# Optimization experiments

Hardware: AMD Instinct MI355X
Metric: run time of the kernel (lower is better)

The kernel has to match this reference:

```python
import jax, jax.numpy as jnp
import numpy as np

B, T, C = 4, 1024, 1024
HEAD_SIZE = 64
H = C // HEAD_SIZE
N_LAYER, LAYER_ID = 24, 12
D_MIX_LORA, D_DECAY_LORA = 32, 64
HEAD_SIZE_DIVISOR = 8
LN_EPS = 1e-5 * HEAD_SIZE_DIVISOR ** 2


def setup_inputs() -> dict:
    key = jax.random.key(0)
    ks = jax.random.split(key, 16)
    x = jax.random.normal(ks[0], (B, T, C), jnp.float32)

    r01 = LAYER_ID / (N_LAYER - 1)          # ratio_0_to_1
    r10 = 1.0 - LAYER_ID / N_LAYER          # ratio_1_to_almost0
    ddd = np.arange(C, dtype=np.float64) / C

    time_maa_x = jnp.asarray((1.0 - ddd ** r10).astype(np.float32))
    time_maa_w = jnp.asarray((1.0 - ddd ** r10).astype(np.float32))
    time_maa_k = jnp.asarray((1.0 - ddd ** r10).astype(np.float32))
    time_maa_v = jnp.asarray((1.0 - (ddd ** r10 + 0.3 * r01)).astype(np.float32))
    time_maa_r = jnp.asarray((1.0 - ddd ** (0.5 * r10)).astype(np.float32))
    time_maa_g = jnp.asarray((1.0 - ddd ** (0.5 * r10)).astype(np.float32))

    n = np.arange(C, dtype=np.float64)
    time_decay = jnp.asarray((-6.0 + 5.0 * (n / (C - 1)) ** (0.7 + 1.3 * r01)).astype(np.float32))
    zigzag = ((n + 1) % 3 - 1) * 0.1
    time_faaaa = jnp.asarray((r01 * (1.0 - n / (C - 1)) + zigzag).astype(np.float32)).reshape(H, HEAD_SIZE)

    u = lambda k, shp: jax.random.uniform(k, shp, jnp.float32, -0.01, 0.01)
    time_maa_w1 = u(ks[1], (C, D_MIX_LORA * 5))   # zeros in orig init; small random for a non-trivial test
    time_maa_w2 = u(ks[2], (5, D_MIX_LORA, C))
    time_decay_w1 = u(ks[3], (C, D_DECAY_LORA))
    time_decay_w2 = u(ks[4], (D_DECAY_LORA, C))

    s = 1.0 / np.sqrt(C)
    Wr = jax.random.normal(ks[5], (C, C), jnp.float32) * s   # stored [in, out]
    Wk = jax.random.normal(ks[6], (C, C), jnp.float32) * s
    Wv = jax.random.normal(ks[7], (C, C), jnp.float32) * s
    Wg = jax.random.normal(ks[8], (C, C), jnp.float32) * s
    Wo = jax.random.normal(ks[9], (C, C), jnp.float32) * s
    ln_w = jnp.ones((C,), jnp.float32)
    ln_b = jnp.zeros((C,), jnp.float32)

    return dict(x=x, time_maa_x=time_maa_x, time_maa_w=time_maa_w, time_maa_k=time_maa_k,
                time_maa_v=time_maa_v, time_maa_r=time_maa_r, time_maa_g=time_maa_g,
                time_maa_w1=time_maa_w1, time_maa_w2=time_maa_w2,
                time_decay=time_decay, time_decay_w1=time_decay_w1, time_decay_w2=time_decay_w2,
                time_faaaa=time_faaaa, Wr=Wr, Wk=Wk, Wv=Wv, Wg=Wg, Wo=Wo, ln_w=ln_w, ln_b=ln_b)


def _wkv6(r, k, v, w, u):
    # r,k,v,w: [B,T,H,N]; u: [H,N]. Data-dependent linear recurrence per head.
    def step(S, inp):               # S: [B,H,N,N] (key dim j, value dim i)
        r_t, k_t, v_t, w_t = inp    # each [B,H,N]
        y = jnp.einsum('bhj,bhji->bhi', r_t, S) \
            + jnp.sum(r_t * u * k_t, axis=-1, keepdims=True) * v_t
        decay = jnp.exp(-jnp.exp(w_t))            # CUDA kernel: w_eff = exp(-exp(w))
        S = decay[..., None] * S + k_t[..., None] * v_t[..., None, :]
        return S, y

    to_t = lambda a: jnp.transpose(a, (1, 0, 2, 3))  # [T,B,H,N]
    S0 = jnp.zeros(r.shape[:1] + (r.shape[2], r.shape[3], r.shape[3]), r.dtype)
    _, ys = jax.lax.scan(step, S0, (to_t(r), to_t(k), to_t(v), to_t(w)))
    return jnp.transpose(ys, (1, 0, 2, 3))            # [B,T,H,N]


def reference(x, time_maa_x, time_maa_w, time_maa_k, time_maa_v, time_maa_r, time_maa_g,
              time_maa_w1, time_maa_w2, time_decay, time_decay_w1, time_decay_w2,
              time_faaaa, Wr, Wk, Wv, Wg, Wo, ln_w, ln_b):
    b, t, c = x.shape
    h, n = H, HEAD_SIZE

    # token shift: ZeroPad2d((0,0,1,-1)) shifts time right by one with zero pad
    xx = jnp.concatenate([jnp.zeros_like(x[:, :1]), x[:, :-1]], axis=1) - x
    xxx = x + xx * time_maa_x
    mix = jnp.tanh(xxx @ time_maa_w1).reshape(b, t, 5, D_MIX_LORA)
    m = jnp.einsum('btsd,sdc->sbtc', mix, time_maa_w2)  # [5,B,T,C]
    xw = x + xx * (time_maa_w + m[0])
    xk = x + xx * (time_maa_k + m[1])
    xv = x + xx * (time_maa_v + m[2])
    xr = x + xx * (time_maa_r + m[3])
    xg = x + xx * (time_maa_g + m[4])

    r = xr @ Wr
    k = xk @ Wk
    v = xv @ Wv
    g = jax.nn.silu(xg @ Wg)
    w = time_decay + jnp.tanh(xw @ time_decay_w1) @ time_decay_w2

    y = _wkv6(r.reshape(b, t, h, n), k.reshape(b, t, h, n),
              v.reshape(b, t, h, n), w.reshape(b, t, h, n), time_faaaa)

    # GroupNorm with n_head groups over channel dim, eps = 1e-5 * divisor^2
    mu = y.mean(-1, keepdims=True)
    var = y.var(-1, keepdims=True)
    yn = ((y - mu) / jnp.sqrt(var + LN_EPS)).reshape(b, t, c) * ln_w + ln_b

    return (yn * g) @ Wo
```

## Files before the change

kernel.cpp:

```cpp
#include <hip/hip_runtime.h>

typedef unsigned short u16;
typedef short short8 __attribute__((ext_vector_type(8)));
typedef short short4v __attribute__((ext_vector_type(4)));
typedef float float4v __attribute__((ext_vector_type(4)));
typedef unsigned uint4v __attribute__((ext_vector_type(4)));

__device__ __forceinline__ float bf2f(u16 h) { return __uint_as_float(((unsigned)h) << 16); }
__device__ __forceinline__ u16 f2bf(float f) {
  unsigned u = __float_as_uint(f);
  unsigned r = (u + 0x7fffu + ((u >> 16) & 1u)) >> 16;
  return (u16)r;
}
__device__ __forceinline__ bool is_f32(const void* probe) {
  return ((const u16*)probe)[0] != 0x3F80;
}
__device__ __forceinline__ float ldin(const void* p, long i, bool f32m) {
  return f32m ? ((const float*)p)[i] : bf2f(((const u16*)p)[i]);
}

typedef __attribute__((address_space(1))) const unsigned int as1_u32;
typedef __attribute__((address_space(3))) unsigned int as3_u32;
__device__ __forceinline__ void gl2lds16(const void* g, void* l) {
  __builtin_amdgcn_global_load_lds((as1_u32*)g, (as3_u32*)l, 16, 0, 0);
}

template <int CTRL>
__device__ __forceinline__ float dpp_add(float x) {
  int s = __builtin_amdgcn_update_dpp(0, __float_as_int(x), CTRL, 0xF, 0xF, true);
  return x + __int_as_float(s);
}

__global__ __launch_bounds__(256) void sentinel_fill(u16* o, long n) {
  long i = (long)blockIdx.x * 256 + threadIdx.x;
  if (i < n) o[i] = 0x42C8;
}

struct TDescArr {
  const void* src[13];
  u16* dst[13];
  int rows[13];
  int cols[13];
  int roff[13];
};

__global__ __launch_bounds__(256) void transpose_all(TDescArr d, const void* probe) {
  bool f32m = is_f32(probe);
  int z = blockIdx.z;
  int rows = d.rows[z], cols = d.cols[z], roff = d.roff[z];
  int bc = blockIdx.x * 32, br = blockIdx.y * 32;
  if (bc >= cols || br >= rows) return;
  const void* src = d.src[z];
  u16* dst = d.dst[z];
  __shared__ u16 tile[32][33];
  int tx = threadIdx.x & 31, ty = threadIdx.x >> 5;
#pragma unroll
  for (int i = 0; i < 32; i += 8)
    tile[ty + i][tx] = f2bf(ldin(src, (long)(roff + br + ty + i) * cols + bc + tx, f32m));
  __syncthreads();
#pragma unroll
  for (int i = 0; i < 32; i += 8)
    dst[(long)(bc + ty + i) * rows + br + tx] = tile[tx][ty + i];
}

__global__ __launch_bounds__(256) void token_shift(const void* __restrict__ x,
                                                   const void* __restrict__ maa_x,
                                                   u16* __restrict__ xxx) {
  bool f32m = is_f32(maa_x);
  long idx = (long)blockIdx.x * 256 + threadIdx.x;
  int c = (int)(idx & 1023);
  int tt = (int)((idx >> 10) & 1023);
  float xv = ldin(x, idx, f32m);
  float xp = tt > 0 ? ldin(x, idx - 1024, f32m) : 0.f;
  xxx[idx] = f2bf(xv + (xp - xv) * ldin(maa_x, c, f32m));
}

template <int EPI>
__global__ __launch_bounds__(256, 2) void gemm_big(const u16* __restrict__ A,
                                                   const u16* __restrict__ Bt,
                                                   void* __restrict__ Cv, int M, int N,
                                                   int K, const void* probe) {
  __shared__ alignas(16) u16 As[128 * 32];
  __shared__ alignas(16) u16 Bs[128 * 32];
  int t = threadIdx.x, lane = t & 63, w = t >> 6;
  int sid = blockIdx.y * gridDim.x + blockIdx.x;
  int per8 = (gridDim.x * gridDim.y) >> 3;
  int L = (sid & 7) * per8 + (sid >> 3);
  int mi = L / gridDim.y, ni = L % gridDim.y;
  int m0 = mi * 128, n0 = ni * 128;
  int wm = (w >> 1) * 64, wn = (w & 1) * 64;
  int lr = lane & 15, lk = lane >> 4;
  float4v acc[4][4];
#pragma unroll
  for (int i = 0; i < 4; i++)
#pragma unroll
    for (int j = 0; j < 4; j++) acc[i][j] = (float4v){0.f, 0.f, 0.f, 0.f};
  const u16* Ag0 = A + (long)(m0 + (t >> 2)) * K + (t & 3) * 8;
  const u16* Ag1 = A + (long)(m0 + 64 + (t >> 2)) * K + (t & 3) * 8;
  const u16* Bg0 = Bt + (long)(n0 + (t >> 2)) * K + (t & 3) * 8;
  const u16* Bg1 = Bt + (long)(n0 + 64 + (t >> 2)) * K + (t & 3) * 8;
  int so = w * 512;
  for (int k0 = 0; k0 < K; k0 += 32) {
    __syncthreads();
    gl2lds16(Ag0 + k0, As + so);
    gl2lds16(Ag1 + k0, As + 2048 + so);
    gl2lds16(Bg0 + k0, Bs + so);
    gl2lds16(Bg1 + k0, Bs + 2048 + so);
    __syncthreads();
    short8 af[4], bfr[4];
#pragma unroll
    for (int i = 0; i < 4; i++)
      af[i] = *(const short8*)(As + (wm + i * 16 + lr) * 32 + lk * 8);
#pragma unroll
    for (int i = 0; i < 4; i++)
      bfr[i] = *(const short8*)(Bs + (wn + i * 16 + lr) * 32 + lk * 8);
#pragma unroll
    for (int mi2 = 0; mi2 < 4; mi2++)
#pragma unroll
      for (int ni2 = 0; ni2 < 4; ni2++)
        acc[mi2][ni2] = __builtin_amdgcn_mfma_f32_16x16x32_bf16(af[mi2], bfr[ni2],
                                                                acc[mi2][ni2], 0, 0, 0);
  }
  bool f32m = (EPI == 2) ? is_f32(probe) : false;
#pragma unroll
  for (int mi2 = 0; mi2 < 4; mi2++) {
#pragma unroll
    for (int ni2 = 0; ni2 < 4; ni2++) {
      int col = n0 + wn + ni2 * 16 + lr;
#pragma unroll
      for (int rr = 0; rr < 4; rr++) {
        long row = m0 + wm + mi2 * 16 + lk * 4 + rr;
        float val = acc[mi2][ni2][rr];
        if (EPI == 1) val = val / (1.f + __expf(-val));
        if (EPI == 2 && f32m) ((float*)Cv)[row * N + col] = val;
        else ((u16*)Cv)[row * N + col] = f2bf(val);
      }
    }
  }
}

template <int EPI0, int EPI1>
__global__ __launch_bounds__(256, 2) void gemm_big2(
    const u16* __restrict__ A0, const u16* __restrict__ Bt0, u16* __restrict__ C0,
    const u16* __restrict__ A1, const u16* __restrict__ Bt1, u16* __restrict__ C1,
    int M, int N, int K) {
  __shared__ alignas(16) u16 As[128 * 32];
  __shared__ alignas(16) u16 Bs[128 * 32];
  int z = blockIdx.z;
  const u16* A = z ? A1 : A0;
  const u16* Bt = z ? Bt1 : Bt0;
  u16* C = z ? C1 : C0;
  int epi = z ? EPI1 : EPI0;
  int t = threadIdx.x, lane = t & 63, w = t >> 6;
  int sid = blockIdx.y * gridDim.x + blockIdx.x;
  int per8 = (gridDim.x * gridDim.y) >> 3;
  int L = (sid & 7) * per8 + (sid >> 3);
  int mi = L / gridDim.y, ni = L % gridDim.y;
  int m0 = mi * 128, n0 = ni * 128;
  int wm = (w >> 1) * 64, wn = (w & 1) * 64;
  int lr = lane & 15, lk = lane >> 4;
  float4v acc[4][4];
#pragma unroll
  for (int i = 0; i < 4; i++)
#pragma unroll
    for (int j = 0; j < 4; j++) acc[i][j] = (float4v){0.f, 0.f, 0.f, 0.f};
  const u16* Ag0 = A + (long)(m0 + (t >> 2)) * K + (t & 3) * 8;
  const u16* Ag1 = A + (long)(m0 + 64 + (t >> 2)) * K + (t & 3) * 8;
  const u16* Bg0 = Bt + (long)(n0 + (t >> 2)) * K + (t & 3) * 8;
  const u16* Bg1 = Bt + (long)(n0 + 64 + (t >> 2)) * K + (t & 3) * 8;
  int so = w * 512;
  for (int k0 = 0; k0 < K; k0 += 32) {
    __syncthreads();
    gl2lds16(Ag0 + k0, As + so);
    gl2lds16(Ag1 + k0, As + 2048 + so);
    gl2lds16(Bg0 + k0, Bs + so);
    gl2lds16(Bg1 + k0, Bs + 2048 + so);
    __syncthreads();
    short8 af[4], bfr[4];
#pragma unroll
    for (int i = 0; i < 4; i++)
      af[i] = *(const short8*)(As + (wm + i * 16 + lr) * 32 + lk * 8);
#pragma unroll
    for (int i = 0; i < 4; i++)
      bfr[i] = *(const short8*)(Bs + (wn + i * 16 + lr) * 32 + lk * 8);
#pragma unroll
    for (int mi2 = 0; mi2 < 4; mi2++)
#pragma unroll
      for (int ni2 = 0; ni2 < 4; ni2++)
        acc[mi2][ni2] = __builtin_amdgcn_mfma_f32_16x16x32_bf16(af[mi2], bfr[ni2],
                                                                acc[mi2][ni2], 0, 0, 0);
  }
#pragma unroll
  for (int mi2 = 0; mi2 < 4; mi2++) {
#pragma unroll
    for (int ni2 = 0; ni2 < 4; ni2++) {
      int col = n0 + wn + ni2 * 16 + lr;
#pragma unroll
      for (int rr = 0; rr < 4; rr++) {
        long row = m0 + wm + mi2 * 16 + lk * 4 + rr;
        float val = acc[mi2][ni2][rr];
        if (epi == 1) val = val / (1.f + __expf(-val));
        C[row * N + col] = f2bf(val);
      }
    }
  }
}

template <int EPI>
__global__ __launch_bounds__(256) void gemm_wave(const u16* __restrict__ A, int lda,
                                                 const u16* __restrict__ Bt,
                                                 u16* __restrict__ C, int ldc,
                                                 float* dA_, float* dB_, int Ntot,
                                                 int K, const void* aux0,
                                                 const void* probe,
                                                 const void* __restrict__ xin) {
  int t = threadIdx.x, lane = t & 63, w = t >> 6;
  int m0 = blockIdx.x * 64 + w * 16;
  int span = Ntot / gridDim.y;
  int col0 = blockIdx.y * span;
  const u16* Bp = Bt + (long)col0 * K;
  int lr = lane & 15, lk = lane >> 4;
  bool f32m = (EPI >= 2) ? is_f32(probe) : false;
  int nt = span >> 4;
  for (int g0 = 0; g0 < nt; g0 += 4) {
    int gc = (nt - g0 < 4) ? (nt - g0) : 4;
    float4v acc[4];
#pragma unroll
    for (int i = 0; i < 4; i++) acc[i] = (float4v){0.f, 0.f, 0.f, 0.f};
    for (int k0 = 0; k0 < K; k0 += 32) {
      short8 a = *(const short8*)(A + (long)(m0 + lr) * lda + k0 + lk * 8);
      for (int gi = 0; gi < gc; gi++) {
        int n0 = (g0 + gi) * 16;
        short8 b = *(const short8*)(Bp + (long)(n0 + lr) * K + k0 + lk * 8);
        acc[gi] = __builtin_amdgcn_mfma_f32_16x16x32_bf16(a, b, acc[gi], 0, 0, 0);
      }
    }
    for (int gi = 0; gi < gc; gi++) {
      int col = col0 + (g0 + gi) * 16 + lr;
      if (EPI == 3) {
        long r0 = m0 + lk * 4;
        float xv4[4];
#pragma unroll
        for (int rr = 0; rr < 4; rr++)
          xv4[rr] = ldin(xin, (r0 + rr) * 1024 + col, f32m);
        float xpv = ((int)(r0 & 1023) > 0) ? ldin(xin, (r0 - 1) * 1024 + col, f32m) : 0.f;
        float mv = ldin(aux0, col, f32m);
#pragma unroll
        for (int rr = 0; rr < 4; rr++) {
          float xv = xv4[rr];
          float xp = (rr == 0) ? xpv : xv4[rr - 1];
          C[(r0 + rr) * 1024 + col] = f2bf(xv + (xp - xv) * (mv + acc[gi][rr]));
        }
      } else {
#pragma unroll
        for (int rr = 0; rr < 4; rr++) {
          long row = m0 + lk * 4 + rr;
          float val = acc[gi][rr];
          if (EPI == 0) {
            C[row * ldc + col] = f2bf(val);
          } else if (EPI == 1) {
            float vv = fminf(fmaxf(val, -15.f), 15.f);
            float e = __expf(2.f * vv);
            C[row * ldc + col] = f2bf((e - 1.f) / (e + 1.f));
          } else if (EPI == 2) {
            float wv = val + ldin(aux0, col, f32m);
            float dv = __expf(-__expf(wv));
            if (row < 2048) dA_[row * 1024 + col] = dv;
            else dB_[(row - 2048) * 1024 + col] = dv;
          }
        }
      }
    }
  }
}

__global__ __launch_bounds__(256) void gemm_wave3_pair(
    const u16* __restrict__ A0, const u16* __restrict__ Bt0, u16* __restrict__ C0,
    const void* __restrict__ maa0, const u16* __restrict__ A1,
    const u16* __restrict__ Bt1, u16* __restrict__ C1,
    const void* __restrict__ maa1, const void* probe,
    const void* __restrict__ xin) {
  int z = blockIdx.z;
  const u16* A = z ? A1 : A0;
  const u16* Bt = z ? Bt1 : Bt0;
  u16* C = z ? C1 : C0;
  const void* maa = z ? maa1 : maa0;
  bool f32m = is_f32(probe);
  int t = threadIdx.x, lane = t & 63, w = t >> 6;
  int m0 = blockIdx.x * 64 + w * 16;
  int col0 = blockIdx.y * 32;
  const u16* Bp = Bt + (long)col0 * 32;
  int lr = lane & 15, lk = lane >> 4;
  float4v acc[2];
  acc[0] = (float4v){0.f, 0.f, 0.f, 0.f};
  acc[1] = (float4v){0.f, 0.f, 0.f, 0.f};
  short8 a = *(const short8*)(A + (long)(m0 + lr) * 160 + lk * 8);
#pragma unroll
  for (int gi = 0; gi < 2; gi++) {
    short8 b = *(const short8*)(Bp + (long)(gi * 16 + lr) * 32 + lk * 8);
    acc[gi] = __builtin_amdgcn_mfma_f32_16x16x32_bf16(a, b, acc[gi], 0, 0, 0);
  }
#pragma unroll
  for (int gi = 0; gi < 2; gi++) {
    int col = col0 + gi * 16 + lr;
    long r0 = m0 + lk * 4;
    float xv4[4];
#pragma unroll
    for (int rr = 0; rr < 4; rr++)
      xv4[rr] = ldin(xin, (r0 + rr) * 1024 + col, f32m);
    float xpv = ((int)(r0 & 1023) > 0) ? ldin(xin, (r0 - 1) * 1024 + col, f32m) : 0.f;
    float mv = ldin(maa, col, f32m);
#pragma unroll
    for (int rr = 0; rr < 4; rr++) {
      float xv = xv4[rr];
      float xp = (rr == 0) ? xpv : xv4[rr - 1];
      C[(r0 + rr) * 1024 + col] = f2bf(xv + (xp - xv) * (mv + acc[gi][rr]));
    }
  }
}

__global__ __launch_bounds__(256) void gemm_n64_tanh(const u16* __restrict__ A,
                                                     const u16* __restrict__ Bt,
                                                     u16* __restrict__ C) {
  int t = threadIdx.x, lane = t & 63, w = t >> 6;
  int m0 = blockIdx.x * 16;
  int n0 = w * 16;
  int lr = lane & 15, lk = lane >> 4;
  float4v acc = (float4v){0.f, 0.f, 0.f, 0.f};
  const u16* Ap = A + (long)(m0 + lr) * 1024;
  const u16* Bp = Bt + (long)(n0 + lr) * 1024;
  for (int k0 = 0; k0 < 1024; k0 += 32) {
    short8 a = *(const short8*)(Ap + k0 + lk * 8);
    short8 b = *(const short8*)(Bp + k0 + lk * 8);
    acc = __builtin_amdgcn_mfma_f32_16x16x32_bf16(a, b, acc, 0, 0, 0);
  }
#pragma unroll
  for (int rr = 0; rr < 4; rr++) {
    long row = m0 + lk * 4 + rr;
    float vv = fminf(fmaxf(acc[rr], -15.f), 15.f);
    float e = __expf(2.f * vv);
    C[row * 64 + n0 + lr] = f2bf((e - 1.f) / (e + 1.f));
  }
}

__global__ __launch_bounds__(256) void wkv6_kernel(
    const u16* __restrict__ r, const u16* __restrict__ k, const u16* __restrict__ v,
    const float* __restrict__ dA_, const float* __restrict__ dB_,
    const void* __restrict__ u_, const void* probe, u16* __restrict__ y) {
  bool f32m = is_f32(probe);
  int bx = blockIdx.x;
  int cb = bx >> 6, bh = bx & 63;
  int b = bh >> 4, h = bh & 15;
  int t = threadIdx.x, lane = t & 63, w = t >> 6;
  int cl = lane >> 3, jq = lane & 7;
  int kp = w * 8 + jq;
  __shared__ alignas(16) uint4v rkd[32][33];
  __shared__ alignas(16) float vsm[8][36];
  __shared__ alignas(16) float ypn[4][8][36];
  float S0 = 0.f, S1 = 0.f;
  float u0 = ldin(u_, h * 64 + 2 * kp, f32m);
  float u1 = ldin(u_, h * 64 + 2 * kp + 1, f32m);
  const long base = ((long)b << 20) + h * 64;
  const float* dgb =
      (b < 2 ? dA_ + (long)b * 1048576 : dB_ + (long)(b - 2) * 1048576) + h * 64;

  int s_tt = t >> 5, s_kp = t & 31;
  int v_tt = t >> 3, v_c = t & 7;

  for (int c0 = 0; c0 < 1024; c0 += 32) {
    {
#pragma unroll
      for (int i = 0; i < 4; i++) {
        int tt = s_tt + i * 8;
        long ro = (long)(c0 + tt) << 10;
        unsigned r2 = *(const unsigned*)(r + base + ro + s_kp * 2);
        unsigned k2 = *(const unsigned*)(k + base + ro + s_kp * 2);
        const float* dp = dgb + ro + s_kp * 2;
        rkd[tt][s_kp] =
            (uint4v){r2, k2, __float_as_uint(dp[0]), __float_as_uint(dp[1])};
      }
      vsm[v_c][v_tt] = bf2f(v[base + ((long)(c0 + v_tt) << 10) + cb * 8 + v_c]);
    }
    __syncthreads();
    float4v vv4;
    float4v yy4;
#pragma unroll
    for (int tt = 0; tt < 32; ++tt) {
      if ((tt & 3) == 0) vv4 = *(const float4v*)&vsm[cl][tt];
      float vt = vv4[tt & 3];
      uint4v q = rkd[tt][kp];
      float r0 = bf2f((u16)(q[0] & 0xffffu)), r1 = bf2f((u16)(q[0] >> 16));
      float k0 = bf2f((u16)(q[1] & 0xffffu)), k1 = bf2f((u16)(q[1] >> 16));
      float d0 = __uint_as_float(q[2]), d1 = __uint_as_float(q[3]);
      float kv0 = k0 * vt, kv1 = k1 * vt;
      float y0 = r0 * fmaf(u0, kv0, S0);
      float y1 = r1 * fmaf(u1, kv1, S1);
      S0 = fmaf(S0, d0, kv0);
      S1 = fmaf(S1, d1, kv1);
      float yy = y0 + y1;
      yy = dpp_add<0xB1>(yy);
      yy = dpp_add<0x4E>(yy);
      yy = dpp_add<0x104>(yy);
      yy4[tt & 3] = yy;
      if ((tt & 3) == 3 && jq == 0)
        *(float4v*)&ypn[w][cl][tt - 3] = yy4;
    }
    __syncthreads();
    {
      int rt = t >> 3, rc = t & 7;
      float s = (ypn[0][rc][rt] + ypn[1][rc][rt]) + (ypn[2][rc][rt] + ypn[3][rc][rt]);
      y[base + ((long)(c0 + rt) << 10) + cb * 8 + rc] = f2bf(s);
    }
    __syncthreads();
  }
}

__global__ __launch_bounds__(256) void gn_gate(const u16* __restrict__ y,
                                               const u16* __restrict__ g,
                                               const void* __restrict__ lnw,
                                               const void* __restrict__ lnb,
                                               const void* probe,
                                               u16* __restrict__ out) {
  bool f32m = is_f32(probe);
  int gid = blockIdx.x * 4 + (threadIdx.x >> 6);
  int lane = threadIdx.x & 63;
  int h = gid & 15;
  long row = gid >> 4;
  long off = row * 1024 + h * 64 + lane;
  float val = bf2f(y[off]);
  float s = val, sq = val * val;
#pragma unroll
  for (int m = 1; m < 64; m <<= 1) {
    s += __shfl_xor(s, m);
    sq += __shfl_xor(sq, m);
  }
  float mean = s * (1.f / 64.f);
  float var = fmaxf(sq * (1.f / 64.f) - mean * mean, 0.f);
  float inv = rsqrtf(var + 6.4e-4f);
  int c = h * 64 + lane;
  float yn = (val - mean) * inv * ldin(lnw, c, f32m) + ldin(lnb, c, f32m);
  out[off] = f2bf(yn * bf2f(g[off]));
}

extern "C" void kernel_launch(void* const* d_in, const int* in_sizes, int n_in,
                              void* d_out, int out_size, void* d_ws, size_t ws_size,
                              hipStream_t stream) {
  const void* x = d_in[0];
  const void* maaX = d_in[1];
  const void* maa_s[5] = {d_in[2], d_in[3], d_in[4], d_in[5], d_in[6]};
  const void* w1 = d_in[7];
  const void* w2 = d_in[8];
  const void* tdec = d_in[9];
  const void* dw1 = d_in[10];
  const void* dw2 = d_in[11];
  const void* faaaa = d_in[12];
  const void* Wr = d_in[13];
  const void* Wk = d_in[14];
  const void* Wv = d_in[15];
  const void* Wg = d_in[16];
  const void* Wo = d_in[17];
  const void* lnw = d_in[18];
  const void* lnb = d_in[19];

  const long oWoT = 4194304;
  const long ow1T = 5242880;
  const long odw1T = 5406720;
  const long odw2T = 5472256;
  const long ow2T = 5537792;
  const long omixb = 5701632;
  const long owtan = 6356992;
  const long oxxxg = 6619136;
  const long omx = 10813440;
  const long orb = 15007744;
  const long okb = 19202048;
  const long ovb = 23396352;
  const long oyb = 27590656;
  const long oend = 31784960;
  const size_t needed = (size_t)oend * 2;

  if (ws_size < needed) {
    sentinel_fill<<<dim3((unsigned)((out_size + 255) / 256)), 256, 0, stream>>>(
        (u16*)d_out, out_size);
    return;
  }

  u16* W = (u16*)d_ws;
  u16* WrT = W;
  u16* WkT = W + 1048576;
  u16* WvT = W + 2097152;
  u16* WgT = W + 3145728;
  u16* WoT = W + oWoT;
  u16* w1T = W + ow1T;
  u16* dw1T = W + odw1T;
  u16* dw2T = W + odw2T;
  u16* w2T = W + ow2T;
  u16* mixb = W + omixb;
  u16* wtan = W + owtan;
  u16* xxxg = W + oxxxg;
  u16* mx = W + omx;
  u16* rbuf = W + orb;
  u16* kbuf = W + okb;
  u16* vbuf = W + ovb;
  u16* ybuf = W + oyb;
  float* dA_ = (float*)W;
  float* dB_ = (float*)(W + omx);
  u16* gated = mx;

  TDescArr td;
  const void* s5[5] = {Wr, Wk, Wv, Wg, Wo};
  u16* t5[5] = {WrT, WkT, WvT, WgT, WoT};
  for (int i = 0; i < 13; i++) td.roff[i] = 0;
  for (int i = 0; i < 5; i++) {
    td.src[i] = s5[i]; td.dst[i] = t5[i]; td.rows[i] = 1024; td.cols[i] = 1024;
  }
  td.src[5] = w1;  td.dst[5] = w1T;  td.rows[5] = 1024; td.cols[5] = 160;
  td.src[6] = dw1; td.dst[6] = dw1T; td.rows[6] = 1024; td.cols[6] = 64;
  td.src[7] = dw2; td.dst[7] = dw2T; td.rows[7] = 64;   td.cols[7] = 1024;
  for (int s = 0; s < 5; s++) {
    td.src[8 + s] = w2;
    td.dst[8 + s] = w2T + s * 1024 * 32;
    td.rows[8 + s] = 32; td.cols[8 + s] = 1024; td.roff[8 + s] = s * 32;
  }

  transpose_all<<<dim3(32, 32, 13), 256, 0, stream>>>(td, maaX);
  token_shift<<<dim3(16384), 256, 0, stream>>>(x, maaX, xxxg);
  gemm_wave<1><<<dim3(64, 10), 256, 0, stream>>>(xxxg, 1024, w1T, mixb, 160, nullptr,
                                                 nullptr, 160, 1024, nullptr, nullptr,
                                                 nullptr);
  gemm_wave3_pair<<<dim3(64, 32, 2), 256, 0, stream>>>(
      mixb + 3 * 32, w2T + 3 * 32768, mx, maa_s[3],
      mixb + 1 * 32, w2T + 1 * 32768, ybuf, maa_s[1], maaX, x);
  gemm_big2<0, 0><<<dim3(32, 8, 2), 256, 0, stream>>>(mx, WrT, rbuf, ybuf, WkT, kbuf,
                                                      4096, 1024, 1024);
  gemm_wave3_pair<<<dim3(64, 32, 2), 256, 0, stream>>>(
      mixb + 2 * 32, w2T + 2 * 32768, mx, maa_s[2],
      mixb + 4 * 32, w2T + 4 * 32768, ybuf, maa_s[4], maaX, x);
  gemm_big2<0, 1><<<dim3(32, 8, 2), 256, 0, stream>>>(mx, WvT, vbuf, ybuf, WgT, xxxg,
                                                      4096, 1024, 1024);
  gemm_wave<3><<<dim3(64, 32), 256, 0, stream>>>(mixb + 0 * 32, 160, w2T + 0 * 32768,
                                                 mx, 1024, nullptr, nullptr, 1024, 32,
                                                 maa_s[0], maaX, x);
  gemm_n64_tanh<<<dim3(256), 256, 0, stream>>>(mx, dw1T, wtan);
  gemm_wave<2><<<dim3(64, 16), 256, 0, stream>>>(wtan, 64, dw2T, nullptr, 0, dA_, dB_,
                                                 1024, 64, tdec, maaX, nullptr);
  wkv6_kernel<<<dim3(512), 256, 0, stream>>>(rbuf, kbuf, vbuf, dA_, dB_, faaaa, maaX,
                                             ybuf);
  gn_gate<<<dim3(16384), 256, 0, stream>>>(ybuf, xxxg, lnw, lnb, maaX, gated);
  gemm_big<2><<<dim3(32, 8), 256, 0, stream>>>(gated, WoT, d_out, 4096, 1024, 1024, maaX);
}
```

Measured before the change: 388.3 us.

## Double GEMM K-tile to 64 with XOR-swizzled LDS and pack WKV math

The shared 128x128 GEMM body is factored into one core routine whose K step grows from 32 to 64. The LDS tile uses an XOR swizzle on the 16-byte chunk index so fragment reads avoid bank conflicts, and half as many barriers run per K. The WKV recurrence is rewritten with two-wide float vectors so the compiler can emit packed FP32 ops, and the bf16 unpack is simplified. The larger LDS tiles (32KB per block) may limit occupancy at two blocks per CU.

After: 378.0 us. 1.03x faster.

```diff
diff --git a/kernel.cpp b/kernel.cpp
--- a/kernel.cpp
+++ b/kernel.cpp
@@ -4,6 +4,7 @@
 typedef short short8 __attribute__((ext_vector_type(8)));
 typedef short short4v __attribute__((ext_vector_type(4)));
 typedef float float4v __attribute__((ext_vector_type(4)));
+typedef float float2v __attribute__((ext_vector_type(2)));
 typedef unsigned uint4v __attribute__((ext_vector_type(4)));
 
 __device__ __forceinline__ float bf2f(u16 h) { return __uint_as_float(((unsigned)h) << 16); }
@@ -76,18 +77,12 @@
 }
 
 template <int EPI>
-__global__ __launch_bounds__(256, 2) void gemm_big(const u16* __restrict__ A,
-                                                   const u16* __restrict__ Bt,
-                                                   void* __restrict__ Cv, int M, int N,
-                                                   int K, const void* probe) {
-  __shared__ alignas(16) u16 As[128 * 32];
-  __shared__ alignas(16) u16 Bs[128 * 32];
+__device__ __forceinline__ void gemm128_core(const u16* __restrict__ A,
+                                             const u16* __restrict__ Bt,
+                                             void* __restrict__ Cv, int N, int K,
+                                             int m0, int n0, u16* As, u16* Bs,
+                                             bool f32m) {
   int t = threadIdx.x, lane = t & 63, w = t >> 6;
-  int sid = blockIdx.y * gridDim.x + blockIdx.x;
-  int per8 = (gridDim.x * gridDim.y) >> 3;
-  int L = (sid & 7) * per8 + (sid >> 3);
-  int mi = L / gridDim.y, ni = L % gridDim.y;
-  int m0 = mi * 128, n0 = ni * 128;
   int wm = (w >> 1) * 64, wn = (w & 1) * 64;
   int lr = lane & 15, lk = lane >> 4;
   float4v acc[4][4];
@@ -95,33 +90,48 @@
   for (int i = 0; i < 4; i++)
 #pragma unroll
     for (int j = 0; j < 4; j++) acc[i][j] = (float4v){0.f, 0.f, 0.f, 0.f};
-  const u16* Ag0 = A + (long)(m0 + (t >> 2)) * K + (t & 3) * 8;
-  const u16* Ag1 = A + (long)(m0 + 64 + (t >> 2)) * K + (t & 3) * 8;
-  const u16* Bg0 = Bt + (long)(n0 + (t >> 2)) * K + (t & 3) * 8;
-  const u16* Bg1 = Bt + (long)(n0 + 64 + (t >> 2)) * K + (t & 3) * 8;
+  int srow = t >> 3;
+  int scol = ((t & 7) ^ (srow & 7)) * 8;
+  const u16* Ag = A + (long)(m0 + srow) * K + scol;
+  const u16* Bg = Bt + (long)(n0 + srow) * K + scol;
   int so = w * 512;
-  for (int k0 = 0; k0 < K; k0 += 32) {
+  for (int k0 = 0; k0 < K; k0 += 64) {
     __syncthreads();
-    gl2lds16(Ag0 + k0, As + so);
-    gl2lds16(Ag1 + k0, As + 2048 + so);
-    gl2lds16(Bg0 + k0, Bs + so);
-    gl2lds16(Bg1 + k0, Bs + 2048 + so);
+#pragma unroll
+    for (int p = 0; p < 4; p++) {
+      gl2lds16(Ag + (long)p * 32 * K + k0, As + p * 2048 + so);
+      gl2lds16(Bg + (long)p * 32 * K + k0, Bs + p * 2048 + so);
+    }
     __syncthreads();
-    short8 af[4], bfr[4];
-#pragma unroll
-    for (int i = 0; i < 4; i++)
-      af[i] = *(const short8*)(As + (wm + i * 16 + lr) * 32 + lk * 8);
-#pragma unroll
-    for (int i = 0; i < 4; i++)
-      bfr[i] = *(const short8*)(Bs + (wn + i * 16 + lr) * 32 + lk * 8);
+    short8 af[4][2], bfr[4][2];
+#pragma unroll
+    for (int i = 0; i < 4; i++) {
+      int R = wm + i * 16 + lr;
+#pragma unroll
+      for (int h = 0; h < 2; h++) {
+        int j = h * 4 + lk;
+        af[i][h] = *(const short8*)(As + R * 64 + (j ^ (R & 7)) * 8);
+      }
+    }
+#pragma unroll
+    for (int i = 0; i < 4; i++) {
+      int R = wn + i * 16 + lr;
+#pragma unroll
+      for (int h = 0; h < 2; h++) {
+        int j = h * 4 + lk;
+        bfr[i][h] = *(const short8*)(Bs + R * 64 + (j ^ (R & 7)) * 8);
+      }
+    }
 #pragma unroll
     for (int mi2 = 0; mi2 < 4; mi2++)
 #pragma unroll
-      for (int ni2 = 0; ni2 < 4; ni2++)
-        acc[mi2][ni2] = __builtin_amdgcn_mfma_f32_16x16x32_bf16(af[mi2], bfr[ni2],
-                                                                acc[mi2][ni2], 0, 0, 0);
-  }
-  bool f32m = (EPI == 2) ? is_f32(probe) : false;
+      for (int ni2 = 0; ni2 < 4; ni2++) {
+        acc[mi2][ni2] = __builtin_amdgcn_mfma_f32_16x16x32_bf16(
+            af[mi2][0], bfr[ni2][0], acc[mi2][ni2], 0, 0, 0);
+        acc[mi2][ni2] = __builtin_amdgcn_mfma_f32_16x16x32_bf16(
+            af[mi2][1], bfr[ni2][1], acc[mi2][ni2], 0, 0, 0);
+      }
+  }
 #pragma unroll
   for (int mi2 = 0; mi2 < 4; mi2++) {
 #pragma unroll
@@ -139,71 +149,37 @@
   }
 }
 
+template <int EPI>
+__global__ __launch_bounds__(256, 2) void gemm_big(const u16* __restrict__ A,
+                                                   const u16* __restrict__ Bt,
+                                                   void* __restrict__ Cv, int M, int N,
+                                                   int K, const void* probe) {
+  __shared__ alignas(16) u16 As[128 * 64];
+  __shared__ alignas(16) u16 Bs[128 * 64];
+  int sid = blockIdx.y * gridDim.x + blockIdx.x;
+  int per8 = (gridDim.x * gridDim.y) >> 3;
+  int L = (sid & 7) * per8 + (sid >> 3);
+  int mi = L / gridDim.y, ni = L % gridDim.y;
+  bool f32m = (EPI == 2) ? is_f32(probe) : false;
+  gemm128_core<EPI>(A, Bt, Cv, N, K, mi * 128, ni * 128, As, Bs, f32m);
+}
+
 template <int EPI0, int EPI1>
 __global__ __launch_bounds__(256, 2) void gemm_big2(
     const u16* __restrict__ A0, const u16* __restrict__ Bt0, u16* __restrict__ C0,
     const u16* __restrict__ A1, const u16* __restrict__ Bt1, u16* __restrict__ C1,
     int M, int N, int K) {
-  __shared__ alignas(16) u16 As[128 * 32];
-  __shared__ alignas(16) u16 Bs[128 * 32];
+  __shared__ alignas(16) u16 As[128 * 64];
+  __shared__ alignas(16) u16 Bs[128 * 64];
   int z = blockIdx.z;
-  const u16* A = z ? A1 : A0;
-  const u16* Bt = z ? Bt1 : Bt0;
-  u16* C = z ? C1 : C0;
-  int epi = z ? EPI1 : EPI0;
-  int t = threadIdx.x, lane = t & 63, w = t >> 6;
   int sid = blockIdx.y * gridDim.x + blockIdx.x;
   int per8 = (gridDim.x * gridDim.y) >> 3;
   int L = (sid & 7) * per8 + (sid >> 3);
   int mi = L / gridDim.y, ni = L % gridDim.y;
-  int m0 = mi * 128, n0 = ni * 128;
-  int wm = (w >> 1) * 64, wn = (w & 1) * 64;
-  int lr = lane & 15, lk = lane >> 4;
-  float4v acc[4][4];
-#pragma unroll
-  for (int i = 0; i < 4; i++)
-#pragma unroll
-    for (int j = 0; j < 4; j++) acc[i][j] = (float4v){0.f, 0.f, 0.f, 0.f};
-  const u16* Ag0 = A + (long)(m0 + (t >> 2)) * K + (t & 3) * 8;
-  const u16* Ag1 = A + (long)(m0 + 64 + (t >> 2)) * K + (t & 3) * 8;
-  const u16* Bg0 = Bt + (long)(n0 + (t >> 2)) * K + (t & 3) * 8;
-  const u16* Bg1 = Bt + (long)(n0 + 64 + (t >> 2)) * K + (t & 3) * 8;
-  int so = w * 512;
-  for (int k0 = 0; k0 < K; k0 += 32) {
-    __syncthreads();
-    gl2lds16(Ag0 + k0, As + so);
-    gl2lds16(Ag1 + k0, As + 2048 + so);
-    gl2lds16(Bg0 + k0, Bs + so);
-    gl2lds16(Bg1 + k0, Bs + 2048 + so);
-    __syncthreads();
-    short8 af[4], bfr[4];
-#pragma unroll
-    for (int i = 0; i < 4; i++)
-      af[i] = *(const short8*)(As + (wm + i * 16 + lr) * 32 + lk * 8);
-#pragma unroll
-    for (int i = 0; i < 4; i++)
-      bfr[i] = *(const short8*)(Bs + (wn + i * 16 + lr) * 32 + lk * 8);
-#pragma unroll
-    for (int mi2 = 0; mi2 < 4; mi2++)
-#pragma unroll
-      for (int ni2 = 0; ni2 < 4; ni2++)
-        acc[mi2][ni2] = __builtin_amdgcn_mfma_f32_16x16x32_bf16(af[mi2], bfr[ni2],
-                                                                acc[mi2][ni2], 0, 0, 0);
-  }
-#pragma unroll
-  for (int mi2 = 0; mi2 < 4; mi2++) {
-#pragma unroll
-    for (int ni2 = 0; ni2 < 4; ni2++) {
-      int col = n0 + wn + ni2 * 16 + lr;
-#pragma unroll
-      for (int rr = 0; rr < 4; rr++) {
-        long row = m0 + wm + mi2 * 16 + lk * 4 + rr;
-        float val = acc[mi2][ni2][rr];
-        if (epi == 1) val = val / (1.f + __expf(-val));
-        C[row * N + col] = f2bf(val);
-      }
-    }
-  }
+  if (z == 0)
+    gemm128_core<EPI0>(A0, Bt0, C0, N, K, mi * 128, ni * 128, As, Bs, false);
+  else
+    gemm128_core<EPI1>(A1, Bt1, C1, N, K, mi * 128, ni * 128, As, Bs, false);
 }
 
 template <int EPI>
@@ -357,9 +333,10 @@
   __shared__ alignas(16) uint4v rkd[32][33];
   __shared__ alignas(16) float vsm[8][36];
   __shared__ alignas(16) float ypn[4][8][36];
-  float S0 = 0.f, S1 = 0.f;
-  float u0 = ldin(u_, h * 64 + 2 * kp, f32m);
-  float u1 = ldin(u_, h * 64 + 2 * kp + 1, f32m);
+  float2v S = (float2v){0.f, 0.f};
+  float2v u2;
+  u2[0] = ldin(u_, h * 64 + 2 * kp, f32m);
+  u2[1] = ldin(u_, h * 64 + 2 * kp + 1, f32m);
   const long base = ((long)b << 20) + h * 64;
   const float* dgb =
       (b < 2 ? dA_ + (long)b * 1048576 : dB_ + (long)(b - 2) * 1048576) + h * 64;
@@ -389,15 +366,18 @@
       if ((tt & 3) == 0) vv4 = *(const float4v*)&vsm[cl][tt];
       float vt = vv4[tt & 3];
       uint4v q = rkd[tt][kp];
-      float r0 = bf2f((u16)(q[0] & 0xffffu)), r1 = bf2f((u16)(q[0] >> 16));
-      float k0 = bf2f((u16)(q[1] & 0xffffu)), k1 = bf2f((u16)(q[1] >> 16));
-      float d0 = __uint_as_float(q[2]), d1 = __uint_as_float(q[3]);
-      float kv0 = k0 * vt, kv1 = k1 * vt;
-      float y0 = r0 * fmaf(u0, kv0, S0);
-      float y1 = r1 * fmaf(u1, kv1, S1);
-      S0 = fmaf(S0, d0, kv0);
-      S1 = fmaf(S1, d1, kv1);
-      float yy = y0 + y1;
+      float2v rv, kv2, dv;
+      rv[0] = __uint_as_float(q[0] << 16);
+      rv[1] = __uint_as_float(q[0] & 0xffff0000u);
+      kv2[0] = __uint_as_float(q[1] << 16);
+      kv2[1] = __uint_as_float(q[1] & 0xffff0000u);
+      dv[0] = __uint_as_float(q[2]);
+      dv[1] = __uint_as_float(q[3]);
+      float2v vt2 = (float2v){vt, vt};
+      float2v kv = kv2 * vt2;
+      float2v y2 = rv * (u2 * kv + S);
+      S = S * dv + kv;
+      float yy = y2[0] + y2[1];
       yy = dpp_add<0xB1>(yy);
       yy = dpp_add<0x4E>(yy);
       yy = dpp_add<0x104>(yy);
```
